# Optimization experiments

Measured on AMD Instinct MI355X. Metric: run time of the kernel, lower is better.

Reference implementation:

```python
import jax, jax.numpy as jnp
import numpy as np

B, F, H, E = 16384, 128, 64, 16


def setup_inputs() -> dict:
    key = jax.random.key(0)
    k_x, k_w1, k_b1, k_w2, k_b2 = jax.random.split(key, 5)
    # Per-feature stacked params: Linear(1,H) -> W1 [F,H], b1 [F,H];
    # Linear(H,E) -> W2 [F,E,H], b2 [F,E]. Scaled like torch default init.
    x = jax.random.normal(k_x, (B, F), dtype=jnp.float32)
    W1 = jax.random.uniform(k_w1, (F, H), jnp.float32, -1.0, 1.0)  # bound = 1/sqrt(in=1)
    b1 = jax.random.uniform(k_b1, (F, H), jnp.float32, -1.0, 1.0)
    bnd = 1.0 / np.sqrt(H)
    W2 = jax.random.uniform(k_w2, (F, E, H), jnp.float32, -bnd, bnd)
    b2 = jax.random.uniform(k_b2, (F, E), jnp.float32, -bnd, bnd)
    return {"x": x, "W1": W1, "b1": b1, "W2": W2, "b2": b2}


def reference(x, W1, b1, W2, b2) -> jnp.ndarray:
    # h[b,f,h] = relu(x[b,f] * W1[f,h] + b1[f,h])   (Linear(1,H) is a scalar-vector product)
    h = jax.nn.relu(x[:, :, None] * W1[None, :, :] + b1[None, :, :])  # [B,F,H]
    # emb[b,f,e] = sum_h h[b,f,h] * W2[f,e,h] + b2[f,e]
    emb = jnp.einsum("bfh,feh->bfe", h, W2) + b2[None, :, :]  # [B,F,E]
    # concat per-feature embeddings along last dim -> [B, F*E]
    return emb.reshape(x.shape[0], -1)
```

## Files before the change

### kernel.cpp

```cpp
#include <hip/hip_runtime.h>


#define F_   128
#define H_   64
#define E_   16
#define NROW 65
#define GRS  32
#define RS   36
#define TPF  (NROW * RS)
#define FPB  4
#define RPI  16
#define ITERS 8
#define BPB  (RPI * ITERS)
#define THREADS 256

typedef float vf4 __attribute__((ext_vector_type(4)));

__global__ __launch_bounds__(64) void build_tables(
    const float* __restrict__ W1, const float* __restrict__ B1,
    const float* __restrict__ W2, const float* __restrict__ B2,
    float* __restrict__ tbl, float* __restrict__ bps)
{
    const int f = blockIdx.x;
    const int h = threadIdx.x;

    __shared__ float ts_raw[H_];
    __shared__ float ts_sorted[H_];
    __shared__ float scS[H_];
    __shared__ float scT[H_];

    const float w1 = W1[f * H_ + h];
    const float bb = B1[f * H_ + h];
    const bool  slope = (w1 != 0.0f);
    const float t   = slope ? (-bb / w1) : __builtin_inff();
    const float sgn = slope ? (w1 > 0.0f ? 1.0f : -1.0f) : 0.0f;
    const bool act0 = (w1 < 0.0f) || (!slope && bb > 0.0f);

    ts_raw[h] = t;
    __syncthreads();
    int rank = 0;
    #pragma unroll
    for (int j = 0; j < H_; ++j) {
        float tj = ts_raw[j];
        rank += (tj < t || (tj == t && j < h)) ? 1 : 0;
    }
    ts_sorted[rank] = t;
    __syncthreads();
    bps[f * H_ + h] = ts_sorted[h];

    for (int e = 0; e < E_; ++e) {
        const float w2 = W2[(f * E_ + e) * H_ + h];
        const float dS = sgn * w1 * w2;
        const float dT = sgn * bb * w2;
        float bS = act0 ? w1 * w2 : 0.0f;
        float bT = act0 ? bb * w2 : 0.0f;
        #pragma unroll
        for (int d = 32; d; d >>= 1) { bS += __shfl_xor(bS, d); bT += __shfl_xor(bT, d); }

        __syncthreads();
        scS[rank] = dS; scT[rank] = dT;
        __syncthreads();
        float vS = scS[h], vT = scT[h];
        #pragma unroll
        for (int d = 1; d < 64; d <<= 1) {
            float uS = __shfl_up(vS, (unsigned)d);
            float uT = __shfl_up(vT, (unsigned)d);
            if (h >= d) { vS += uS; vT += uT; }
        }
        const float b2v = B2[f * E_ + e];
        float* row = tbl + ((size_t)f * NROW + (h + 1)) * GRS;
        row[e]      = bS + vS;
        row[E_ + e] = bT + vT + b2v;
        if (h == 0) {
            float* r0 = tbl + (size_t)f * NROW * GRS;
            r0[e]      = bS;
            r0[E_ + e] = bT + b2v;
        }
    }
}

__global__ __launch_bounds__(THREADS, 4) void embed_main(
    const float* __restrict__ x, const float* __restrict__ tbl,
    const float* __restrict__ bps, float* __restrict__ out)
{
    __shared__ float lt[FPB * TPF];

    const int tid = threadIdx.x;
    const int f0  = blockIdx.y * FPB;

    const int   eq   = tid & 3;
    const int   fl   = (tid >> 2) & 3;
    const int   rloc = tid >> 4;
    const int   f    = f0 + fl;
    const int bbase  = blockIdx.x * BPB;

    float xs[ITERS];
    #pragma unroll
    for (int it = 0; it < ITERS; ++it)
        xs[it] = x[(size_t)(bbase + it * RPI + rloc) * F_ + f];

    float4 bp[16];
    #pragma unroll
    for (int i = 0; i < 16; ++i)
        bp[i] = *(const float4*)(bps + (size_t)f * H_ + 4 * i);

    for (int i = tid; i < FPB * NROW * 8; i += THREADS) {
        int fl2 = i / (NROW * 8); int r = i - fl2 * (NROW * 8);
        int k = r >> 3; int c4 = (r & 7) << 2;
        float4 v = *(const float4*)(tbl + ((size_t)(f0 + fl2) * NROW + k) * GRS + c4);
        *(float4*)(lt + fl2 * TPF + k * RS + c4) = v;
    }
    __syncthreads();

    const float* myt = lt + fl * TPF;

    #pragma unroll
    for (int it = 0; it < ITERS; ++it) {
        const int   b  = bbase + it * RPI + rloc;
        const float xv = xs[it];
        int k0 = 0, k1 = 0, k2 = 0, k3 = 0;
        #pragma unroll
        for (int i = 0; i < 16; ++i) {
            k0 += (bp[i].x <= xv) ? 1 : 0;
            k1 += (bp[i].y <= xv) ? 1 : 0;
            k2 += (bp[i].z <= xv) ? 1 : 0;
            k3 += (bp[i].w <= xv) ? 1 : 0;
        }
        const int k = (k0 + k1) + (k2 + k3);
        const float* row = myt + k * RS + eq * 4;
        float4 S = *(const float4*)(row);
        float4 T = *(const float4*)(row + E_);
        vf4 o;
        o.x = fmaf(S.x, xv, T.x);
        o.y = fmaf(S.y, xv, T.y);
        o.z = fmaf(S.z, xv, T.z);
        o.w = fmaf(S.w, xv, T.w);
        vf4* op = (vf4*)(out + (size_t)b * (F_ * E_) + f * E_ + eq * 4);
        __builtin_nontemporal_store(o, op);
    }
}

extern "C" void kernel_launch(void* const* d_in, const int* in_sizes, int n_in,
                              void* d_out, int out_size, void* d_ws, size_t ws_size,
                              hipStream_t stream) {
    const float* x  = (const float*)d_in[0];
    const float* W1 = (const float*)d_in[1];
    const float* b1 = (const float*)d_in[2];
    const float* W2 = (const float*)d_in[3];
    const float* b2 = (const float*)d_in[4];
    float* out = (float*)d_out;
    const int B = in_sizes[0] / F_;

    float* tbl = (float*)d_ws;
    float* bps = tbl + (size_t)F_ * NROW * GRS;

    build_tables<<<F_, 64, 0, stream>>>(W1, b1, W2, b2, tbl, bps);
    dim3 grid(B / BPB, F_ / FPB);
    embed_main<<<grid, THREADS, 0, stream>>>(x, tbl, bps, out);
}
```

Before: 195.1 us.

## Parallelize table build over E, split breakpoint search across lanes, drop LDS table

```diff
diff --git a/kernel.cpp b/kernel.cpp
--- a/kernel.cpp
+++ b/kernel.cpp
@@ -6,8 +6,6 @@
 #define E_   16
 #define NROW 65
 #define GRS  32
-#define RS   36
-#define TPF  (NROW * RS)
 #define FPB  4
 #define RPI  16
 #define ITERS 8
@@ -22,6 +20,7 @@
     float* __restrict__ tbl, float* __restrict__ bps)
 {
     const int f = blockIdx.x;
+    const int e = blockIdx.y;
     const int h = threadIdx.x;
 
     __shared__ float ts_raw[H_];
@@ -46,36 +45,33 @@
     }
     ts_sorted[rank] = t;
     __syncthreads();
-    bps[f * H_ + h] = ts_sorted[h];
+    if (e == 0) bps[f * H_ + h] = ts_sorted[h];
 
-    for (int e = 0; e < E_; ++e) {
-        const float w2 = W2[(f * E_ + e) * H_ + h];
-        const float dS = sgn * w1 * w2;
-        const float dT = sgn * bb * w2;
-        float bS = act0 ? w1 * w2 : 0.0f;
-        float bT = act0 ? bb * w2 : 0.0f;
-        #pragma unroll
-        for (int d = 32; d; d >>= 1) { bS += __shfl_xor(bS, d); bT += __shfl_xor(bT, d); }
+    const float w2 = W2[(f * E_ + e) * H_ + h];
+    const float dS = sgn * w1 * w2;
+    const float dT = sgn * bb * w2;
+    float bS = act0 ? w1 * w2 : 0.0f;
+    float bT = act0 ? bb * w2 : 0.0f;
+    #pragma unroll
+    for (int d = 32; d; d >>= 1) { bS += __shfl_xor(bS, d); bT += __shfl_xor(bT, d); }
 
-        __syncthreads();
-        scS[rank] = dS; scT[rank] = dT;
-        __syncthreads();
-        float vS = scS[h], vT = scT[h];
-        #pragma unroll
-        for (int d = 1; d < 64; d <<= 1) {
-            float uS = __shfl_up(vS, (unsigned)d);
-            float uT = __shfl_up(vT, (unsigned)d);
-            if (h >= d) { vS += uS; vT += uT; }
-        }
-        const float b2v = B2[f * E_ + e];
-        float* row = tbl + ((size_t)f * NROW + (h + 1)) * GRS;
-        row[e]      = bS + vS;
-        row[E_ + e] = bT + vT + b2v;
-        if (h == 0) {
-            float* r0 = tbl + (size_t)f * NROW * GRS;
-            r0[e]      = bS;
-            r0[E_ + e] = bT + b2v;
-        }
+    scS[rank] = dS; scT[rank] = dT;
+    __syncthreads();
+    float vS = scS[h], vT = scT[h];
+    #pragma unroll
+    for (int d = 1; d < 64; d <<= 1) {
+        float uS = __shfl_up(vS, (unsigned)d);
+        float uT = __shfl_up(vT, (unsigned)d);
+        if (h >= d) { vS += uS; vT += uT; }
+    }
+    const float b2v = B2[f * E_ + e];
+    float* row = tbl + ((size_t)f * NROW + (h + 1)) * GRS;
+    row[e]      = bS + vS;
+    row[E_ + e] = bT + vT + b2v;
+    if (h == 0) {
+        float* r0 = tbl + (size_t)f * NROW * GRS;
+        r0[e]      = bS;
+        r0[E_ + e] = bT + b2v;
     }
 }
 
@@ -83,8 +79,6 @@
     const float* __restrict__ x, const float* __restrict__ tbl,
     const float* __restrict__ bps, float* __restrict__ out)
 {
-    __shared__ float lt[FPB * TPF];
-
     const int tid = threadIdx.x;
     const int f0  = blockIdx.y * FPB;
 
@@ -99,35 +93,28 @@
     for (int it = 0; it < ITERS; ++it)
         xs[it] = x[(size_t)(bbase + it * RPI + rloc) * F_ + f];
 
-    float4 bp[16];
+    float4 bp[4];
     #pragma unroll
-    for (int i = 0; i < 16; ++i)
-        bp[i] = *(const float4*)(bps + (size_t)f * H_ + 4 * i);
+    for (int i = 0; i < 4; ++i)
+        bp[i] = *(const float4*)(bps + (size_t)f * H_ + eq * 16 + 4 * i);
 
-    for (int i = tid; i < FPB * NROW * 8; i += THREADS) {
-        int fl2 = i / (NROW * 8); int r = i - fl2 * (NROW * 8);
-        int k = r >> 3; int c4 = (r & 7) << 2;
-        float4 v = *(const float4*)(tbl + ((size_t)(f0 + fl2) * NROW + k) * GRS + c4);
-        *(float4*)(lt + fl2 * TPF + k * RS + c4) = v;
-    }
-    __syncthreads();
-
-    const float* myt = lt + fl * TPF;
+    const float* ftbl = tbl + (size_t)f * NROW * GRS;
 
     #pragma unroll
     for (int it = 0; it < ITERS; ++it) {
         const int   b  = bbase + it * RPI + rloc;
         const float xv = xs[it];
-        int k0 = 0, k1 = 0, k2 = 0, k3 = 0;
+        int c = 0;
         #pragma unroll
-        for (int i = 0; i < 16; ++i) {
-            k0 += (bp[i].x <= xv) ? 1 : 0;
-            k1 += (bp[i].y <= xv) ? 1 : 0;
-            k2 += (bp[i].z <= xv) ? 1 : 0;
-            k3 += (bp[i].w <= xv) ? 1 : 0;
+        for (int i = 0; i < 4; ++i) {
+            c += (bp[i].x <= xv) ? 1 : 0;
+            c += (bp[i].y <= xv) ? 1 : 0;
+            c += (bp[i].z <= xv) ? 1 : 0;
+            c += (bp[i].w <= xv) ? 1 : 0;
         }
-        const int k = (k0 + k1) + (k2 + k3);
-        const float* row = myt + k * RS + eq * 4;
+        c += __shfl_xor(c, 1);
+        c += __shfl_xor(c, 2);
+        const float* row = ftbl + (size_t)c * GRS + eq * 4;
         float4 S = *(const float4*)(row);
         float4 T = *(const float4*)(row + E_);
         vf4 o;
@@ -154,7 +141,7 @@
     float* tbl = (float*)d_ws;
     float* bps = tbl + (size_t)F_ * NROW * GRS;
 
-    build_tables<<<F_, 64, 0, stream>>>(W1, b1, W2, b2, tbl, bps);
+    build_tables<<<dim3(F_, E_), 64, 0, stream>>>(W1, b1, W2, b2, tbl, bps);
     dim3 grid(B / BPB, F_ / FPB);
     embed_main<<<grid, THREADS, 0, stream>>>(x, tbl, bps, out);
 }
```

New measurement: 167.0 us. 14.4% less time.
